# Kernel optimization log

Hardware: AMD Instinct MI355X
Metric: run time of the kernel (lower is better)

## Reference

```python
import jax, jax.numpy as jnp
import numpy as np

VOC, EDIM, HDIM, SSZ, SDIM, SDEPTH, PAD = 32000, 256, 256, 128, 128, 2, 0
N, BSZ = 64, 32
T = 2 * N - 1  # 127
N_ACTS = 2  # push, pop


def _linear(key, out_d, in_d):
    k1, k2 = jax.random.split(key)
    return (jax.random.normal(k1, (out_d, in_d), jnp.float32) * 0.02,
            jax.random.normal(k2, (out_d,), jnp.float32) * 0.02)


def setup_inputs() -> dict:
    key = jax.random.key(0)
    ks = jax.random.split(key, 9)
    emb_W = jax.random.normal(ks[0], (VOC, EDIM), jnp.float32) * 0.02
    emb_W = emb_W.at[PAD].set(0.0)  # padding_idx row is zero in torch
    W_e2h, b_e2h = _linear(ks[1], HDIM, EDIM)
    W_s2h, b_s2h = _linear(ks[2], HDIM, SDIM * SDEPTH)
    W_h2h, b_h2h = _linear(ks[3], HDIM, HDIM)
    W_h2i, b_h2i = _linear(ks[4], N_ACTS + 1, HDIM)
    W_h2s, b_h2s = _linear(ks[5], SDIM, HDIM)
    W_s2u, b_s2u = _linear(ks[6], SDIM, SDIM * SDEPTH)
    empty_elem = jax.random.normal(ks[7], (1, SDIM), jnp.float32) * 0.02
    inputs = jax.random.randint(ks[8], (N, BSZ), 0, VOC)
    return dict(inputs=inputs, emb_W=emb_W, W_e2h=W_e2h, b_e2h=b_e2h,
                W_s2h=W_s2h, b_s2h=b_s2h, W_h2h=W_h2h, b_h2h=b_h2h,
                W_h2i=W_h2i, b_h2i=b_h2i, W_h2s=W_h2s, b_h2s=b_h2s,
                W_s2u=W_s2u, b_s2u=b_s2u, empty_elem=empty_elem)


def _srnn(inputs, emb_W, W_e2h, b_e2h, W_s2h, b_s2h, W_h2h, b_h2h,
          W_h2i, b_h2i, W_h2s, b_h2s, W_s2u, b_s2u, empty_elem):
    bsz = inputs.shape[1]
    embs = emb_W[inputs]                                        # [N, bsz, edim]
    pads = jnp.broadcast_to(emb_W[PAD], (T - N, bsz, EDIM))     # padded tail
    buf0 = jnp.concatenate([embs, pads], axis=0)                # [T, bsz, edim]
    hid0 = jnp.zeros((bsz, HDIM), jnp.float32)
    stack0 = jnp.broadcast_to(empty_elem, (bsz, SSZ, SDIM))

    def step(carry, t):
        hid, stack, buf = carry
        tops = stack[:, :SDEPTH, :].reshape(bsz, SDEPTH * SDIM)
        inp = buf[t]                                            # [bsz, edim]
        ihid = inp @ W_e2h.T + b_e2h + tops @ W_s2h.T + b_s2h
        hid = jax.nn.relu(hid @ W_h2h.T + b_h2h + ihid)
        inst = ihid @ W_h2i.T + b_h2i                           # [bsz, 3]
        act = jax.nn.softmax(inst[:, :N_ACTS], axis=-1)
        gamma = 1.0 + jnp.log1p(jnp.exp(inst[:, N_ACTS:]))      # [bsz, 1]
        a = act ** gamma
        a = a / (jnp.sum(a, axis=-1, keepdims=True) + 1e-16)    # sharpened acts
        p_push, p_pop = a[:, :1], a[:, 1:]                      # [bsz, 1]
        # buffer update: pop shifts the whole buffer down one slot along time
        buf_pop = jnp.concatenate([jnp.zeros_like(buf[:1]), buf[:-1]], axis=0)
        buf = p_push[None] * buf + p_pop[None] * buf_pop        # [1,bsz,1] bcast
        push_val = jax.nn.relu(hid @ W_h2s.T + b_h2s)           # [bsz, sdim]
        u_val = jax.nn.relu(tops @ W_s2u.T + b_s2u)             # [bsz, sdim]
        z = jnp.zeros((bsz, 1, SDIM), jnp.float32)
        # W_push (shift down by 1) as an index roll
        stack_push = jnp.concatenate([z, stack[:, :-1, :]], axis=1)
        stack_push = stack_push.at[:, 0, :].add(push_val)
        # W_pop = shift up by SDEPTH, then W_push = shift down by 1
        up = jnp.concatenate([stack[:, SDEPTH:, :],
                              jnp.zeros((bsz, SDEPTH, SDIM), jnp.float32)], axis=1)
        stack_pop = jnp.concatenate([z, up[:, :-1, :]], axis=1)
        stack_pop = stack_pop.at[:, 0, :].add(u_val)
        stack_pop = stack_pop.at[:, SSZ - SDEPTH + 1:, :].add(empty_elem[0])
        stack = p_push[:, :, None] * stack_push + p_pop[:, :, None] * stack_pop
        return (hid, stack, buf), (hid, a, stack[:, 0, :])

    (hid, stack, _), (outputs, acts, top_elems) = jax.lax.scan(
        step, (hid0, stack0, buf0), jnp.arange(T))
    return outputs, hid, stack, acts, top_elems


def reference(inputs, emb_W, W_e2h, b_e2h, W_s2h, b_s2h, W_h2h, b_h2h,
              W_h2i, b_h2i, W_h2s, b_h2s, W_s2u, b_s2u, empty_elem):
    return _srnn(inputs, emb_W, W_e2h, b_e2h, W_s2h, b_s2h, W_h2h, b_h2h,
                 W_h2i, b_h2i, W_h2s, b_h2s, W_s2u, b_s2u, empty_elem)
```

## Files before the change

### kernel.cpp

```cpp
#include <hip/hip_runtime.h>
#include <stdint.h>
#include <math.h>


#define T_STEPS 127

#define OUT_OFF   0
#define HID_OFF   1040384
#define STACK_OFF 1048576
#define ACTS_OFF  1572864
#define TE_OFF    1580992

#define E2H_OFF_U 131072

typedef _Float16 h2 __attribute__((ext_vector_type(2)));

__device__ __forceinline__ unsigned packh2(float a, float b){
  h2 v; v.x = (_Float16)a; v.y = (_Float16)b;
  return __builtin_bit_cast(unsigned, v);
}
__device__ __forceinline__ float h2loF(unsigned u){ h2 v = __builtin_bit_cast(h2,u); return (float)v.x; }
__device__ __forceinline__ float h2hiF(unsigned u){ h2 v = __builtin_bit_cast(h2,u); return (float)v.y; }

#if __has_builtin(__builtin_amdgcn_fdot2)
__device__ __forceinline__ float fdot2(unsigned a, unsigned b, float c){
  return __builtin_amdgcn_fdot2(__builtin_bit_cast(h2,a), __builtin_bit_cast(h2,b), c, false);
}
#else
__device__ __forceinline__ float fdot2(unsigned a, unsigned b, float c){
  return c + h2loF(a)*h2loF(b) + h2hiF(a)*h2hiF(b);
}
#endif

#define BAR() asm volatile("s_waitcnt lgkmcnt(0)\n\ts_barrier" ::: "memory")

#define CHOFF(u) (12*((u)>>3) + ((u)&7))

__global__ void prep_pack(const float* __restrict__ We2h, const float* __restrict__ Ws2h,
                          const float* __restrict__ Wh2h, const float* __restrict__ Wh2s,
                          const float* __restrict__ Ws2u, uint4* __restrict__ out4){
  int gid = blockIdx.x*256 + threadIdx.x;
  const float* src;
  if (gid < 16384){
    int i = gid >> 10, t_ = gid & 1023;
    const float* S = (t_ < 512) ? Ws2h : Wh2h;
    int r = t_ & 511, jp = r >> 2, ks = r & 3;
    int j = 2*jp + (i >> 3);
    int k0 = ks*64 + (i & 7)*8;
    src = S + j*256 + k0;
  } else if (gid < 20480){
    int l = gid - 16384, i = l >> 10, t_ = l & 1023;
    int jr = t_ >> 4, kb = t_ & 15;
    int j = 2*jr + (i >> 1);
    int k0 = kb*16 + (i & 1)*8;
    src = Wh2s + j*256 + k0;
  } else if (gid < 24576){
    int l = gid - 20480, i = l >> 10, t_ = l & 1023;
    int jr = t_ >> 4, kb = t_ & 15;
    int j = 2*jr + (i >> 1);
    int k0 = kb*16 + (i & 1)*8;
    src = Ws2u + j*256 + k0;
  } else {
    int l = gid - 24576;
    int i8 = l >> 8, j = l & 255;
    src = We2h + j*256 + i8*8;
  }
  uint4 r4;
  r4.x = packh2(src[0], src[1]); r4.y = packh2(src[2], src[3]);
  r4.z = packh2(src[4], src[5]); r4.w = packh2(src[6], src[7]);
  out4[gid] = r4;
}

__global__ void prep_e2h(const int* __restrict__ inputs, const float* __restrict__ embW,
                         const uint4* __restrict__ w04, unsigned* __restrict__ e2hpk){
  __shared__ float emb[8][256];
  int tid = threadIdx.x;
  int r2 = blockIdx.x >> 3, bg = blockIdx.x & 7;
  for (int q=0;q<8;q++){
    int rr = q >> 2, bb = q & 3;
    int tok = inputs[(2*r2+rr)*32 + bg*4+bb];
    emb[q][tid] = embW[tok*256 + tid];
  }
  __syncthreads();
  float acc[8] = {0.f,0.f,0.f,0.f,0.f,0.f,0.f,0.f};
  for (int i8=0;i8<32;i8++){
    uint4 u = w04[i8*256 + tid];
    unsigned uu[4] = {u.x,u.y,u.z,u.w};
    #pragma unroll
    for (int c=0;c<4;c++){
      float lo = h2loF(uu[c]), hi = h2hiF(uu[c]);
      int k = i8*8 + c*2;
      #pragma unroll
      for (int q=0;q<8;q++)
        acc[q] += emb[q][k]*lo + emb[q][k+1]*hi;
    }
  }
  int base = (bg*4)*8192 + r2*256 + tid;
  #pragma unroll
  for (int bb=0;bb<4;bb++)
    e2hpk[base + bb*8192] = packh2(acc[bb], acc[4+bb]);
}

__global__ __attribute__((amdgpu_flat_work_group_size(1024,1024), amdgpu_waves_per_eu(4,4)))
void srnn_main(const uint4* __restrict__ ws4, const unsigned* __restrict__ wsu,
               const float* __restrict__ b_e2h, const float* __restrict__ b_s2h,
               const float* __restrict__ b_h2h, const float* __restrict__ Wh2i,
               const float* __restrict__ b_h2i, const float* __restrict__ b_h2s,
               const float* __restrict__ b_s2u, const float* __restrict__ empty_el,
               float* __restrict__ out)
{
  __shared__ __align__(16) float    stk_s[128*128];
  __shared__ __align__(16) unsigned e2h_s[32*258];
  __shared__ __align__(16) unsigned s_pk[192];
  __shared__ __align__(16) unsigned hid_pk[192];
  __shared__ __align__(16) float    pv_s[128], uv_s[128];
  __shared__ __align__(16) float    accih[256], acchp[256];
  __shared__ __align__(16) float    emptyf_s[128];
  __shared__ float    wbuf[2][192];
  __shared__ unsigned pkwc[32];
  __shared__ float    partsum[12];
  __shared__ float    pp_s, pq_s;

  const int tid = threadIdx.x;
  const int b   = blockIdx.x;
  const int aside = tid >> 9;
  const int ar  = tid & 511;
  const int ajp = ar >> 2;
  const int aks = ar & 3;
  const int jr  = tid >> 4;
  const int ksb = tid & 15;
  const int g   = tid >> 6;
  const int cp  = tid & 63;

  uint4 w1r[16], w3r[4], w2r[4];
  #pragma unroll
  for (int i=0;i<16;i++) w1r[i] = ws4[i*1024 + tid];
  #pragma unroll
  for (int i=0;i<4;i++)  w3r[i] = ws4[16384 + i*1024 + tid];
  #pragma unroll
  for (int i=0;i<4;i++)  w2r[i] = ws4[20480 + i*1024 + tid];

  float bA0=0.f, bA1=0.f;
  if (aks==0){
    int j0 = 2*ajp;
    if (aside==0){ bA0 = b_e2h[j0]+b_s2h[j0]; bA1 = b_e2h[j0+1]+b_s2h[j0+1]; }
    else         { bA0 = b_h2h[j0];           bA1 = b_h2h[j0+1]; }
  }
  float bH0=0.f,bH1=0.f,bU0=0.f,bU1=0.f;
  if (ksb==0){ bH0=b_h2s[2*jr]; bH1=b_h2s[2*jr+1]; bU0=b_s2u[2*jr]; bU1=b_s2u[2*jr+1]; }
  float rW0=0.f,rW1=0.f,rW2=0.f;
  if (tid<256){ rW0=Wh2i[tid]; rW1=Wh2i[256+tid]; rW2=Wh2i[512+tid]; }
  const float bi0=b_h2i[0], bi1=b_h2i[1], bi2=b_h2i[2];

  const unsigned* e2hg = wsu + E2H_OFF_U + b*8192;
  #pragma unroll
  for (int q=0;q<8;q++){
    int idx = q*1024 + tid;
    e2h_s[(idx>>8)*258 + (idx&255)] = e2hg[idx];
  }
  {
    float2 e2 = *(const float2*)&empty_el[2*cp];
    #pragma unroll
    for (int j=0;j<8;j++)
      *(float2*)&stk_s[(8*g+j)*128 + 2*cp] = e2;
  }
  if (tid < 128){
    emptyf_s[tid] = empty_el[tid];
    hid_pk[CHOFF(tid)] = 0u;
    int cu = tid & 63;
    s_pk[CHOFF(tid)] = packh2(empty_el[2*cu], empty_el[2*cu+1]);
  }
  if (tid < 192){ wbuf[0][tid] = (tid==64)?1.f:0.f; wbuf[1][tid]=0.f; }
  if (tid < 32)  pkwc[tid] = (tid==0)? packh2(1.f,0.f) : 0u;
  __syncthreads();

  int cur = 0;
  for (int t=0;t<T_STEPS;++t){
    {
      const unsigned* act  = aside ? hid_pk : s_pk;
      const unsigned* actB = act + 48*aks;
      float x0 = 0.f, x1 = 0.f;
      if (aside==0){
        #pragma unroll
        for (int q=0;q<8;q++){
          int r2 = aks*8 + q;
          unsigned cw = pkwc[r2];
          uint2 e = *(const uint2*)&e2h_s[r2*258 + 2*ajp];
          x0 = fdot2(cw, e.x, x0);
          x1 = fdot2(cw, e.y, x1);
        }
      }
      #pragma unroll
      for (int i=0;i<8;i++){
        uint4 A  = *(const uint4*)(actB + 12*(i>>1) + 4*(i&1));
        uint4 Wa = w1r[i], Wb = w1r[8+i];
        x0 = fdot2(A.x,Wa.x,x0); x0 = fdot2(A.y,Wa.y,x0);
        x0 = fdot2(A.z,Wa.z,x0); x0 = fdot2(A.w,Wa.w,x0);
        x1 = fdot2(A.x,Wb.x,x1); x1 = fdot2(A.y,Wb.y,x1);
        x1 = fdot2(A.z,Wb.z,x1); x1 = fdot2(A.w,Wb.w,x1);
      }
      x0 += __shfl_xor(x0,1); x0 += __shfl_xor(x0,2);
      x1 += __shfl_xor(x1,1); x1 += __shfl_xor(x1,2);
      if (aks==0){
        float* dst = aside ? acchp : accih;
        *(float2*)&dst[2*ajp] = make_float2(x0 + bA0, x1 + bA1);
      }
    }
    BAR();

    if (tid < 128){
      float2 ih2 = *(const float2*)&accih[2*tid];
      float2 hp2 = *(const float2*)&acchp[2*tid];
      float hn0 = fmaxf(ih2.x+hp2.x, 0.f);
      float hn1 = fmaxf(ih2.y+hp2.y, 0.f);
      hid_pk[CHOFF(tid)] = packh2(hn0,hn1);
      *(float2*)&out[OUT_OFF + t*8192 + b*256 + 2*tid] = make_float2(hn0,hn1);
      if (t==T_STEPS-1) *(float2*)&out[HID_OFF + b*256 + 2*tid] = make_float2(hn0,hn1);
    }
    if (tid < 256){
      float v = accih[tid];
      float p0=v*rW0, p1=v*rW1, p2=v*rW2;
      #pragma unroll
      for (int o=32;o>=1;o>>=1){ p0+=__shfl_xor(p0,o); p1+=__shfl_xor(p1,o); p2+=__shfl_xor(p2,o); }
      if ((tid&63)==0){ int w=tid>>6; partsum[w*3]=p0; partsum[w*3+1]=p1; partsum[w*3+2]=p2; }
    }
    BAR();

    if (tid < 64){
      float i0 = bi0+partsum[0]+partsum[3]+partsum[6]+partsum[9];
      float i1 = bi1+partsum[1]+partsum[4]+partsum[7]+partsum[10];
      float gi = bi2+partsum[2]+partsum[5]+partsum[8]+partsum[11];
      float mx = fmaxf(i0,i1);
      float e0 = expf(i0-mx), e1 = expf(i1-mx);
      float inv = 1.f/(e0+e1);
      float act0 = e0*inv, act1 = e1*inv;
      float gamma = 1.f + log1pf(expf(gi));
      float A0 = powf(act0,gamma), A1 = powf(act1,gamma);
      float sden = A0+A1+1e-16f;
      float ppv = A0/sden, pqv = A1/sden;
      if (tid==0){
        pp_s = ppv; pq_s = pqv;
        *(float2*)&out[ACTS_OFF + t*64 + b*2] = make_float2(ppv,pqv);
      }
    }

    {
      const uint4* hptr = (const uint4*)(hid_pk + 12*ksb);
      const uint4* sptr = (const uint4*)(s_pk   + 12*ksb);
      uint4 H0 = hptr[0], H1 = hptr[1];
      uint4 S0 = sptr[0], S1 = sptr[1];
      float h0=0.f,h1=0.f,u0=0.f,u1=0.f;
      h0=fdot2(H0.x,w3r[0].x,h0); h0=fdot2(H0.y,w3r[0].y,h0); h0=fdot2(H0.z,w3r[0].z,h0); h0=fdot2(H0.w,w3r[0].w,h0);
      h0=fdot2(H1.x,w3r[1].x,h0); h0=fdot2(H1.y,w3r[1].y,h0); h0=fdot2(H1.z,w3r[1].z,h0); h0=fdot2(H1.w,w3r[1].w,h0);
      h1=fdot2(H0.x,w3r[2].x,h1); h1=fdot2(H0.y,w3r[2].y,h1); h1=fdot2(H0.z,w3r[2].z,h1); h1=fdot2(H0.w,w3r[2].w,h1);
      h1=fdot2(H1.x,w3r[3].x,h1); h1=fdot2(H1.y,w3r[3].y,h1); h1=fdot2(H1.z,w3r[3].z,h1); h1=fdot2(H1.w,w3r[3].w,h1);
      u0=fdot2(S0.x,w2r[0].x,u0); u0=fdot2(S0.y,w2r[0].y,u0); u0=fdot2(S0.z,w2r[0].z,u0); u0=fdot2(S0.w,w2r[0].w,u0);
      u0=fdot2(S1.x,w2r[1].x,u0); u0=fdot2(S1.y,w2r[1].y,u0); u0=fdot2(S1.z,w2r[1].z,u0); u0=fdot2(S1.w,w2r[1].w,u0);
      u1=fdot2(S0.x,w2r[2].x,u1); u1=fdot2(S0.y,w2r[2].y,u1); u1=fdot2(S0.z,w2r[2].z,u1); u1=fdot2(S0.w,w2r[2].w,u1);
      u1=fdot2(S1.x,w2r[3].x,u1); u1=fdot2(S1.y,w2r[3].y,u1); u1=fdot2(S1.z,w2r[3].z,u1); u1=fdot2(S1.w,w2r[3].w,u1);
      #pragma unroll
      for (int o=8;o>=1;o>>=1){
        h0+=__shfl_xor(h0,o); h1+=__shfl_xor(h1,o);
        u0+=__shfl_xor(u0,o); u1+=__shfl_xor(u1,o);
      }
      if (ksb==0){
        pv_s[2*jr]   = fmaxf(h0+bH0,0.f);
        pv_s[2*jr+1] = fmaxf(h1+bH1,0.f);
        uv_s[2*jr]   = fmaxf(u0+bU0,0.f);
        uv_s[2*jr+1] = fmaxf(u1+bU1,0.f);
      }
    }
    BAR();
    const float pp = pp_s, pq = pq_s;

    {
      float2 w[10];
      #pragma unroll
      for (int k=0;k<10;k++){
        int r = 8*g - 1 + k;
        if (r >= 0 && r <= 127)
          w[k] = *(const float2*)&stk_s[r*128 + 2*cp];
      }
      if (g == 15) w[9] = *(const float2*)&emptyf_s[2*cp];
      float2 pv2 = make_float2(0.f,0.f), uv2 = make_float2(0.f,0.f);
      if (g == 0){ pv2 = *(const float2*)&pv_s[2*cp]; uv2 = *(const float2*)&uv_s[2*cp]; }
      float2 nn[8];
      #pragma unroll
      for (int j=0;j<8;j++){
        nn[j].x = pp*w[j].x + pq*w[j+2].x;
        nn[j].y = pp*w[j].y + pq*w[j+2].y;
      }
      if (g == 0){
        nn[0].x = pp*pv2.x + pq*uv2.x;
        nn[0].y = pp*pv2.y + pq*uv2.y;
      }
      if (tid < 128){
        int k = 64+tid;
        wbuf[cur^1][k] = pp*wbuf[cur][k] + pq*wbuf[cur][k-1];
      } else if (tid < 160){
        int r2 = tid-128;
        int k1 = 65 + t - 2*r2;
        float wa = wbuf[cur][k1], wb2 = wbuf[cur][k1-1], wc2 = wbuf[cur][k1-2];
        pkwc[r2] = packh2(pp*wa+pq*wb2, pp*wb2+pq*wc2);
      }
      BAR();
      #pragma unroll
      for (int j=0;j<8;j++)
        *(float2*)&stk_s[(8*g+j)*128 + 2*cp] = nn[j];
      if (g == 0){
        *(float2*)&out[TE_OFF + t*4096 + b*128 + 2*cp] = nn[0];
        s_pk[CHOFF(cp)]      = packh2(nn[0].x, nn[0].y);
        s_pk[CHOFF(64+cp)]   = packh2(nn[1].x, nn[1].y);
      }
    }
    BAR();
    cur ^= 1;
  }

  #pragma unroll
  for (int j=0;j<8;j++){
    int r = 8*g + j;
    *(float2*)&out[STACK_OFF + b*16384 + r*128 + 2*cp] =
      *(const float2*)&stk_s[r*128 + 2*cp];
  }
}

extern "C" void kernel_launch(void* const* d_in, const int* in_sizes, int n_in,
                              void* d_out, int out_size, void* d_ws, size_t ws_size,
                              hipStream_t stream){
  const int*   inputs = (const int*)d_in[0];
  const float* embW   = (const float*)d_in[1];
  const float* We2h   = (const float*)d_in[2];
  const float* b_e2h  = (const float*)d_in[3];
  const float* Ws2h   = (const float*)d_in[4];
  const float* b_s2h  = (const float*)d_in[5];
  const float* Wh2h   = (const float*)d_in[6];
  const float* b_h2h  = (const float*)d_in[7];
  const float* Wh2i   = (const float*)d_in[8];
  const float* b_h2i  = (const float*)d_in[9];
  const float* Wh2s   = (const float*)d_in[10];
  const float* b_h2s  = (const float*)d_in[11];
  const float* Ws2u   = (const float*)d_in[12];
  const float* b_s2u  = (const float*)d_in[13];
  const float* empty  = (const float*)d_in[14];
  unsigned* wsu = (unsigned*)d_ws;

  prep_pack<<<dim3(128), dim3(256), 0, stream>>>(We2h, Ws2h, Wh2h, Wh2s, Ws2u, (uint4*)wsu);
  prep_e2h<<<dim3(256), dim3(256), 0, stream>>>(inputs, embW, ((const uint4*)wsu)+24576, wsu + E2H_OFF_U);
  srnn_main<<<dim3(32), dim3(1024), 0, stream>>>((const uint4*)wsu, (const unsigned*)wsu,
                                                 b_e2h, b_s2h, b_h2h, Wh2i, b_h2i,
                                                 b_h2s, b_s2u, empty, (float*)d_out);
}
```

Baseline: 897.2 us.

## Fold action softmax into sigmoid, single-wave logits, and repartition h2s/s2u matvec

Computes the instruction logits in a single wave from weights staged in shared memory, which drops the cross-wave partial-sum exchange. The softmax plus power normalisation is rewritten algebraically as a sigmoid of gamma*(i0-i1), evaluated with hardware exp2/log2/rcp intrinsics in place of expf/powf/log1pf. The h2s and s2u matvecs are repacked so that each thread handles one of the two matrices with 8-lane reductions instead of 16-lane ones, and the action work now runs concurrently with the hidden-state update. The sigmoid form drops the 1e-16 epsilon and uses approximate transcendentals, so results may shift slightly in precision.

```diff
diff --git a/kernel.cpp b/kernel.cpp
--- a/kernel.cpp
+++ b/kernel.cpp
@@ -11,6 +11,7 @@
 #define ACTS_OFF  1572864
 #define TE_OFF    1580992
 
+#define WB_OFF 16384
 #define E2H_OFF_U 131072
 
 typedef _Float16 h2 __attribute__((ext_vector_type(2)));
@@ -30,6 +31,22 @@
 __device__ __forceinline__ float fdot2(unsigned a, unsigned b, float c){
   return c + h2loF(a)*h2loF(b) + h2hiF(a)*h2hiF(b);
 }
+#endif
+
+#if __has_builtin(__builtin_amdgcn_exp2f)
+#define EXP2F(x) __builtin_amdgcn_exp2f(x)
+#else
+#define EXP2F(x) exp2f(x)
+#endif
+#if __has_builtin(__builtin_amdgcn_logf)
+#define LOG2F(x) __builtin_amdgcn_logf(x)
+#else
+#define LOG2F(x) log2f(x)
+#endif
+#if __has_builtin(__builtin_amdgcn_rcpf)
+#define RCPF(x) __builtin_amdgcn_rcpf(x)
+#else
+#define RCPF(x) (1.f/(x))
 #endif
 
 #define BAR() asm volatile("s_waitcnt lgkmcnt(0)\n\ts_barrier" ::: "memory")
@@ -48,18 +65,14 @@
     int j = 2*jp + (i >> 3);
     int k0 = ks*64 + (i & 7)*8;
     src = S + j*256 + k0;
-  } else if (gid < 20480){
-    int l = gid - 16384, i = l >> 10, t_ = l & 1023;
-    int jr = t_ >> 4, kb = t_ & 15;
-    int j = 2*jr + (i >> 1);
-    int k0 = kb*16 + (i & 1)*8;
-    src = Wh2s + j*256 + k0;
   } else if (gid < 24576){
-    int l = gid - 20480, i = l >> 10, t_ = l & 1023;
-    int jr = t_ >> 4, kb = t_ & 15;
-    int j = 2*jr + (i >> 1);
-    int k0 = kb*16 + (i & 1)*8;
-    src = Ws2u + j*256 + k0;
+    int l = gid - 16384;
+    int i = l >> 10, t_ = l & 1023;
+    const float* S = (t_ < 512) ? Wh2s : Ws2u;
+    int tt = t_ & 511;
+    int j  = 2*(tt >> 3) + (i >> 2);
+    int k0 = (tt & 7)*32 + (i & 3)*8;
+    src = S + j*256 + k0;
   } else {
     int l = gid - 24576;
     int i8 = l >> 8, j = l & 255;
@@ -116,9 +129,9 @@
   __shared__ __align__(16) float    pv_s[128], uv_s[128];
   __shared__ __align__(16) float    accih[256], acchp[256];
   __shared__ __align__(16) float    emptyf_s[128];
+  __shared__ __align__(16) float    whi_s[768];
   __shared__ float    wbuf[2][192];
   __shared__ unsigned pkwc[32];
-  __shared__ float    partsum[12];
   __shared__ float    pp_s, pq_s;
 
   const int tid = threadIdx.x;
@@ -127,18 +140,16 @@
   const int ar  = tid & 511;
   const int ajp = ar >> 2;
   const int aks = ar & 3;
-  const int jr  = tid >> 4;
-  const int ksb = tid & 15;
+  const int pB  = tid >> 3;
+  const int kB  = tid & 7;
   const int g   = tid >> 6;
   const int cp  = tid & 63;
 
-  uint4 w1r[16], w3r[4], w2r[4];
+  uint4 w1r[16], wBr[8];
   #pragma unroll
   for (int i=0;i<16;i++) w1r[i] = ws4[i*1024 + tid];
   #pragma unroll
-  for (int i=0;i<4;i++)  w3r[i] = ws4[16384 + i*1024 + tid];
-  #pragma unroll
-  for (int i=0;i<4;i++)  w2r[i] = ws4[20480 + i*1024 + tid];
+  for (int i=0;i<8;i++)  wBr[i] = ws4[WB_OFF + i*1024 + tid];
 
   float bA0=0.f, bA1=0.f;
   if (aks==0){
@@ -146,10 +157,11 @@
     if (aside==0){ bA0 = b_e2h[j0]+b_s2h[j0]; bA1 = b_e2h[j0+1]+b_s2h[j0+1]; }
     else         { bA0 = b_h2h[j0];           bA1 = b_h2h[j0+1]; }
   }
-  float bH0=0.f,bH1=0.f,bU0=0.f,bU1=0.f;
-  if (ksb==0){ bH0=b_h2s[2*jr]; bH1=b_h2s[2*jr+1]; bU0=b_s2u[2*jr]; bU1=b_s2u[2*jr+1]; }
-  float rW0=0.f,rW1=0.f,rW2=0.f;
-  if (tid<256){ rW0=Wh2i[tid]; rW1=Wh2i[256+tid]; rW2=Wh2i[512+tid]; }
+  float bB0=0.f, bB1=0.f;
+  if (kB==0){
+    if (pB < 64){ bB0 = b_h2s[2*pB];      bB1 = b_h2s[2*pB+1]; }
+    else        { bB0 = b_s2u[2*(pB-64)]; bB1 = b_s2u[2*(pB-64)+1]; }
+  }
   const float bi0=b_h2i[0], bi1=b_h2i[1], bi2=b_h2i[2];
 
   const unsigned* e2hg = wsu + E2H_OFF_U + b*8192;
@@ -170,6 +182,7 @@
     int cu = tid & 63;
     s_pk[CHOFF(tid)] = packh2(empty_el[2*cu], empty_el[2*cu+1]);
   }
+  if (tid < 768) whi_s[tid] = Wh2i[tid];
   if (tid < 192){ wbuf[0][tid] = (tid==64)?1.f:0.f; wbuf[1][tid]=0.f; }
   if (tid < 32)  pkwc[tid] = (tid==0)? packh2(1.f,0.f) : 0u;
   __syncthreads();
@@ -208,66 +221,61 @@
     }
     BAR();
 
-    if (tid < 128){
-      float2 ih2 = *(const float2*)&accih[2*tid];
-      float2 hp2 = *(const float2*)&acchp[2*tid];
+    if (tid < 64){
+      float4 av = *(const float4*)&accih[4*tid];
+      float4 q0 = *(const float4*)&whi_s[      4*tid];
+      float4 q1 = *(const float4*)&whi_s[256 + 4*tid];
+      float4 q2 = *(const float4*)&whi_s[512 + 4*tid];
+      float p0 = av.x*q0.x + av.y*q0.y + av.z*q0.z + av.w*q0.w;
+      float p1 = av.x*q1.x + av.y*q1.y + av.z*q1.z + av.w*q1.w;
+      float p2 = av.x*q2.x + av.y*q2.y + av.z*q2.z + av.w*q2.w;
+      #pragma unroll
+      for (int o=1;o<=32;o<<=1){
+        p0 += __shfl_xor(p0,o); p1 += __shfl_xor(p1,o); p2 += __shfl_xor(p2,o);
+      }
+      if (tid==0){
+        float i0 = bi0+p0, i1 = bi1+p1, gi = bi2+p2;
+        float gamma = 1.f + 0.6931471806f*LOG2F(1.f + EXP2F(1.442695041f*gi));
+        float z = 1.442695041f*gamma*(i0 - i1);
+        float ppv = RCPF(1.f + EXP2F(-z));
+        float pqv = 1.f - ppv;
+        pp_s = ppv; pq_s = pqv;
+        *(float2*)&out[ACTS_OFF + t*64 + b*2] = make_float2(ppv,pqv);
+      }
+    }
+    if (tid >= 64 && tid < 192){
+      int hl = tid - 64;
+      float2 ih2 = *(const float2*)&accih[2*hl];
+      float2 hp2 = *(const float2*)&acchp[2*hl];
       float hn0 = fmaxf(ih2.x+hp2.x, 0.f);
       float hn1 = fmaxf(ih2.y+hp2.y, 0.f);
-      hid_pk[CHOFF(tid)] = packh2(hn0,hn1);
-      *(float2*)&out[OUT_OFF + t*8192 + b*256 + 2*tid] = make_float2(hn0,hn1);
-      if (t==T_STEPS-1) *(float2*)&out[HID_OFF + b*256 + 2*tid] = make_float2(hn0,hn1);
-    }
-    if (tid < 256){
-      float v = accih[tid];
-      float p0=v*rW0, p1=v*rW1, p2=v*rW2;
-      #pragma unroll
-      for (int o=32;o>=1;o>>=1){ p0+=__shfl_xor(p0,o); p1+=__shfl_xor(p1,o); p2+=__shfl_xor(p2,o); }
-      if ((tid&63)==0){ int w=tid>>6; partsum[w*3]=p0; partsum[w*3+1]=p1; partsum[w*3+2]=p2; }
+      hid_pk[CHOFF(hl)] = packh2(hn0,hn1);
+      *(float2*)&out[OUT_OFF + t*8192 + b*256 + 2*hl] = make_float2(hn0,hn1);
+      if (t==T_STEPS-1) *(float2*)&out[HID_OFF + b*256 + 2*hl] = make_float2(hn0,hn1);
     }
     BAR();
 
-    if (tid < 64){
-      float i0 = bi0+partsum[0]+partsum[3]+partsum[6]+partsum[9];
-      float i1 = bi1+partsum[1]+partsum[4]+partsum[7]+partsum[10];
-      float gi = bi2+partsum[2]+partsum[5]+partsum[8]+partsum[11];
-      float mx = fmaxf(i0,i1);
-      float e0 = expf(i0-mx), e1 = expf(i1-mx);
-      float inv = 1.f/(e0+e1);
-      float act0 = e0*inv, act1 = e1*inv;
-      float gamma = 1.f + log1pf(expf(gi));
-      float A0 = powf(act0,gamma), A1 = powf(act1,gamma);
-      float sden = A0+A1+1e-16f;
-      float ppv = A0/sden, pqv = A1/sden;
-      if (tid==0){
-        pp_s = ppv; pq_s = pqv;
-        *(float2*)&out[ACTS_OFF + t*64 + b*2] = make_float2(ppv,pqv);
-      }
-    }
-
     {
-      const uint4* hptr = (const uint4*)(hid_pk + 12*ksb);
-      const uint4* sptr = (const uint4*)(s_pk   + 12*ksb);
-      uint4 H0 = hptr[0], H1 = hptr[1];
-      uint4 S0 = sptr[0], S1 = sptr[1];
-      float h0=0.f,h1=0.f,u0=0.f,u1=0.f;
-      h0=fdot2(H0.x,w3r[0].x,h0); h0=fdot2(H0.y,w3r[0].y,h0); h0=fdot2(H0.z,w3r[0].z,h0); h0=fdot2(H0.w,w3r[0].w,h0);
-      h0=fdot2(H1.x,w3r[1].x,h0); h0=fdot2(H1.y,w3r[1].y,h0); h0=fdot2(H1.z,w3r[1].z,h0); h0=fdot2(H1.w,w3r[1].w,h0);
-      h1=fdot2(H0.x,w3r[2].x,h1); h1=fdot2(H0.y,w3r[2].y,h1); h1=fdot2(H0.z,w3r[2].z,h1); h1=fdot2(H0.w,w3r[2].w,h1);
-      h1=fdot2(H1.x,w3r[3].x,h1); h1=fdot2(H1.y,w3r[3].y,h1); h1=fdot2(H1.z,w3r[3].z,h1); h1=fdot2(H1.w,w3r[3].w,h1);
-      u0=fdot2(S0.x,w2r[0].x,u0); u0=fdot2(S0.y,w2r[0].y,u0); u0=fdot2(S0.z,w2r[0].z,u0); u0=fdot2(S0.w,w2r[0].w,u0);
-      u0=fdot2(S1.x,w2r[1].x,u0); u0=fdot2(S1.y,w2r[1].y,u0); u0=fdot2(S1.z,w2r[1].z,u0); u0=fdot2(S1.w,w2r[1].w,u0);
-      u1=fdot2(S0.x,w2r[2].x,u1); u1=fdot2(S0.y,w2r[2].y,u1); u1=fdot2(S0.z,w2r[2].z,u1); u1=fdot2(S0.w,w2r[2].w,u1);
-      u1=fdot2(S1.x,w2r[3].x,u1); u1=fdot2(S1.y,w2r[3].y,u1); u1=fdot2(S1.z,w2r[3].z,u1); u1=fdot2(S1.w,w2r[3].w,u1);
-      #pragma unroll
-      for (int o=8;o>=1;o>>=1){
-        h0+=__shfl_xor(h0,o); h1+=__shfl_xor(h1,o);
-        u0+=__shfl_xor(u0,o); u1+=__shfl_xor(u1,o);
-      }
-      if (ksb==0){
-        pv_s[2*jr]   = fmaxf(h0+bH0,0.f);
-        pv_s[2*jr+1] = fmaxf(h1+bH1,0.f);
-        uv_s[2*jr]   = fmaxf(u0+bU0,0.f);
-        uv_s[2*jr+1] = fmaxf(u1+bU1,0.f);
+      const unsigned* srcB = (pB < 64) ? hid_pk : s_pk;
+      const uint4* cA0 = (const uint4*)(srcB + 24*kB);
+      const uint4* cA1 = (const uint4*)(srcB + 24*kB + 12);
+      uint4 A0 = cA0[0], A1 = cA0[1];
+      uint4 A2 = cA1[0], A3 = cA1[1];
+      float y0=0.f, y1=0.f;
+      y0=fdot2(A0.x,wBr[0].x,y0); y0=fdot2(A0.y,wBr[0].y,y0); y0=fdot2(A0.z,wBr[0].z,y0); y0=fdot2(A0.w,wBr[0].w,y0);
+      y0=fdot2(A1.x,wBr[1].x,y0); y0=fdot2(A1.y,wBr[1].y,y0); y0=fdot2(A1.z,wBr[1].z,y0); y0=fdot2(A1.w,wBr[1].w,y0);
+      y0=fdot2(A2.x,wBr[2].x,y0); y0=fdot2(A2.y,wBr[2].y,y0); y0=fdot2(A2.z,wBr[2].z,y0); y0=fdot2(A2.w,wBr[2].w,y0);
+      y0=fdot2(A3.x,wBr[3].x,y0); y0=fdot2(A3.y,wBr[3].y,y0); y0=fdot2(A3.z,wBr[3].z,y0); y0=fdot2(A3.w,wBr[3].w,y0);
+      y1=fdot2(A0.x,wBr[4].x,y1); y1=fdot2(A0.y,wBr[4].y,y1); y1=fdot2(A0.z,wBr[4].z,y1); y1=fdot2(A0.w,wBr[4].w,y1);
+      y1=fdot2(A1.x,wBr[5].x,y1); y1=fdot2(A1.y,wBr[5].y,y1); y1=fdot2(A1.z,wBr[5].z,y1); y1=fdot2(A1.w,wBr[5].w,y1);
+      y1=fdot2(A2.x,wBr[6].x,y1); y1=fdot2(A2.y,wBr[6].y,y1); y1=fdot2(A2.z,wBr[6].z,y1); y1=fdot2(A2.w,wBr[6].w,y1);
+      y1=fdot2(A3.x,wBr[7].x,y1); y1=fdot2(A3.y,wBr[7].y,y1); y1=fdot2(A3.z,wBr[7].z,y1); y1=fdot2(A3.w,wBr[7].w,y1);
+      y0 += __shfl_xor(y0,1); y0 += __shfl_xor(y0,2); y0 += __shfl_xor(y0,4);
+      y1 += __shfl_xor(y1,1); y1 += __shfl_xor(y1,2); y1 += __shfl_xor(y1,4);
+      if (kB==0){
+        float v0 = fmaxf(y0+bB0,0.f), v1 = fmaxf(y1+bB1,0.f);
+        if (pB < 64) *(float2*)&pv_s[2*pB]      = make_float2(v0,v1);
+        else         *(float2*)&uv_s[2*(pB-64)] = make_float2(v0,v1);
       }
     }
     BAR();
```

Result: faster. 843.2 us (-6.0%).
